# Optimization experiments

Hardware: AMD Instinct MI355X
Metric: run time of the kernel (lower is better)

Reference implementation:

```python
import jax, jax.numpy as jnp
import numpy as np

B, T = 32, 1000
NN, NB, CTX = 512, 16, 64
EMB = 256
DCAT = 3 * EMB
H, L = 256, 4
PN, PB = 512, 2
S, V = 8, 64


def setup_inputs() -> dict:
    key = jax.random.key(0)
    ks = jax.random.split(key, 20)
    r = lambda i, shape, sc=1.0: jax.random.normal(ks[i], shape, dtype=jnp.float32) * sc
    nu_log = jnp.log(-jnp.log(jax.random.uniform(ks[8], (L, H), minval=0.5, maxval=0.95)))
    inp = {
        'neural_input': r(0, (B, T, NN)),
        'behavior_input': r(1, (B, T, NB)),
        'session_id': jax.random.randint(ks[2], (B,), 0, V),
        'subject_id': jax.random.randint(ks[3], (B,), 0, S),
        'session_table': r(4, (V, CTX), 0.02),
        'neural_W': r(5, (S, EMB, NN), 1.0 / np.sqrt(NN)),
        'neural_b': jnp.zeros((S, EMB), jnp.float32),
        'behavior_W': r(6, (S, EMB, NB), 1.0 / np.sqrt(NB)),
        'behavior_b': jnp.zeros((S, EMB), jnp.float32),
        'ctx_W': r(7, (EMB, CTX), 1.0 / np.sqrt(CTX)),
        'ctx_b': jnp.zeros((EMB,), jnp.float32),
        'nu_log': nu_log,
        'theta_log': jnp.log(jax.random.uniform(ks[9], (L, H), minval=1e-4, maxval=6.283)),
        'gamma_log': 0.5 * jnp.log1p(-jnp.exp(-2.0 * jnp.exp(nu_log))),
        'B_re': r(10, (L, H, DCAT), 1.0 / np.sqrt(2 * DCAT)),
        'B_im': r(11, (L, H, DCAT), 1.0 / np.sqrt(2 * DCAT)),
        'C_re': r(12, (L, DCAT, H), 1.0 / np.sqrt(H)),
        'C_im': r(13, (L, DCAT, H), 1.0 / np.sqrt(H)),
        'D_skip': r(14, (L, DCAT)),
        'dec_n_W': r(15, (S, PN, DCAT), 1.0 / np.sqrt(DCAT)),
        'dec_n_b': jnp.zeros((S, PN), jnp.float32),
        'dec_b_W': r(16, (S, PB, DCAT), 1.0 / np.sqrt(DCAT)),
        'dec_b_b': jnp.zeros((S, PB), jnp.float32),
    }
    return inp


def _lru(u, nu_log, theta_log, gamma_log, B_re, B_im, C_re, C_im, D_skip):
    # Linear Recurrent Unit: complex diagonal recurrence x_t = lam*x_{t-1} + gamma*B u_t
    lam = jnp.exp(-jnp.exp(nu_log) + 1j * jnp.exp(theta_log))  # [H]
    g = jnp.exp(gamma_log)[:, None]
    Bu = (jnp.einsum('bti,hi->bth', u, B_re * g)
          + 1j * jnp.einsum('bti,hi->bth', u, B_im * g))  # [B,T,H] complex

    def step(x, bu_t):
        x = lam * x + bu_t
        return x, x

    x0 = jnp.zeros((u.shape[0], nu_log.shape[0]), jnp.complex64)
    _, xs = jax.lax.scan(step, x0, jnp.swapaxes(Bu, 0, 1))
    xs = jnp.swapaxes(xs, 0, 1)  # [B,T,H]
    y = jnp.einsum('bth,oh->bto', xs, C_re + 1j * C_im).real + D_skip * u
    return y


def _forward(neural_input, behavior_input, session_table, neural_W, neural_b,
             behavior_W, behavior_b, ctx_W, ctx_b, nu_log, theta_log, gamma_log,
             B_re, B_im, C_re, C_im, D_skip, dec_n_W, dec_n_b, dec_b_W, dec_b_b,
             session_id, subject_id):
    act = jax.nn.relu
    Bsz, Ts, _ = neural_input.shape
    # session-token embedding -> context embedder (Linear is per-timestep, so embed once then broadcast)
    ctx = act(session_table[session_id] @ ctx_W.T + ctx_b)  # [B,EMB]
    ctx = jnp.broadcast_to(ctx[:, None, :], (Bsz, Ts, ctx.shape[-1]))
    # subject-routed embedders: gather per-sample weights, one batched GEMM
    en = act(jnp.einsum('btf,bef->bte', neural_input, neural_W[subject_id])
             + neural_b[subject_id][:, None, :])
    eb = act(jnp.einsum('btf,bef->bte', behavior_input, behavior_W[subject_id])
             + behavior_b[subject_id][:, None, :])
    h = jnp.concatenate([en, eb, ctx], axis=-1)  # [B,T,3*EMB]
    for l in range(nu_log.shape[0]):
        h = _lru(h, nu_log[l], theta_log[l], gamma_log[l],
                 B_re[l], B_im[l], C_re[l], C_im[l], D_skip[l])
    # subject-routed decoders
    pred_n = jax.nn.softplus(jnp.einsum('btd,bod->bto', h, dec_n_W[subject_id])
                             + dec_n_b[subject_id][:, None, :])
    pred_b = (jnp.einsum('btd,bod->bto', h, dec_b_W[subject_id])
              + dec_b_b[subject_id][:, None, :])
    return pred_n, pred_b


def reference(neural_input, behavior_input, session_id, subject_id, session_table,
              neural_W, neural_b, behavior_W, behavior_b, ctx_W, ctx_b,
              nu_log, theta_log, gamma_log, B_re, B_im, C_re, C_im, D_skip,
              dec_n_W, dec_n_b, dec_b_W, dec_b_b):
    return _forward(neural_input, behavior_input, session_table, neural_W, neural_b,
                    behavior_W, behavior_b, ctx_W, ctx_b, nu_log, theta_log, gamma_log,
                    B_re, B_im, C_re, C_im, D_skip, dec_n_W, dec_n_b, dec_b_W, dec_b_b,
                    session_id, subject_id)
```

## Files before the change

kernel.cpp:

```cpp
#include <hip/hip_runtime.h>

typedef __bf16 bf16;
typedef __bf16 bf16x8 __attribute__((ext_vector_type(8)));
typedef float f32x4 __attribute__((ext_vector_type(4)));

#define AS1 __attribute__((address_space(1)))
#define AS3 __attribute__((address_space(3)))

__device__ __forceinline__ void gll16(const void* g, void* l) {
    __builtin_amdgcn_global_load_lds((const AS1 void*)g, (AS3 void*)l, 16, 0, 0);
}

template<int EPI>
__global__ __launch_bounds__(512, 2)
void gemm_kern(const bf16* __restrict__ Abase, long long aBstride, int lda,
               const bf16* __restrict__ Wbase, long long wSstride,
               const float* __restrict__ biasBase, int biasStride,
               void* __restrict__ Cbase, long long cBstride, int ldc,
               const float* __restrict__ dskip,
               const bf16* __restrict__ Ubase, long long uBstride,
               const int* __restrict__ subj,
               int M, int K, int nbn)
{
    __shared__ char smem[147456];

    const int tid = threadIdx.x;
    const int lane = tid & 63;
    const int wid = tid >> 6;
    const int wm = wid >> 1, wn = wid & 1;
    const int l15 = lane & 15, lhi = lane >> 4;
    const int sw7 = l15 & 7;

    const int nwg = gridDim.x;
    const int bid = blockIdx.x;
    const int q = nwg >> 3, r = nwg & 7;
    const int xcd = bid & 7;
    const int sw = xcd * q + (xcd < r ? xcd : r) + (bid >> 3);
    const int m0 = (sw / nbn) * 256;
    const int n0 = (sw % nbn) * 128;

    const int b = blockIdx.z;
    const int s = subj ? subj[b] : 0;
    const bf16* A = Abase + (size_t)b * aBstride;
    const bf16* W = Wbase + (size_t)s * wSstride;
    const float* bias = biasBase ? biasBase + (size_t)s * biasStride : nullptr;
    const bf16* U = Ubase ? Ubase + (size_t)b * uBstride : nullptr;
    const size_t coff = (size_t)b * cBstride;
    const int Mc = M - 1;

    f32x4 acc[4][4];
    #pragma unroll
    for (int i = 0; i < 4; ++i)
        #pragma unroll
        for (int j = 0; j < 4; ++j)
            acc[i][j] = f32x4{0.f, 0.f, 0.f, 0.f};

    int rA[4], rB[4];
    #pragma unroll
    for (int f = 0; f < 4; ++f) {
        rA[f] = (wm*64 + f*16 + l15) * 128;
        rB[f] = (wn*64 + f*16 + l15) * 128;
    }

    const int sub  = tid >> 3;
    const int slot = tid & 7;
    const int ldsw = (wid << 10);

    auto stage = [&](int kt, char* buf) {
        #pragma unroll
        for (int c = 0; c < 4; ++c) {
            const int row = c*64 + sub;
            const int gk = (kt << 6) + ((slot ^ (row & 7)) << 3);
            int ar = m0 + row; if (ar > Mc) ar = Mc;
            gll16(A + (size_t)ar * lda + gk, buf + c*8192 + ldsw);
        }
        #pragma unroll
        for (int c = 0; c < 2; ++c) {
            const int row = c*64 + sub;
            const int gk = (kt << 6) + ((slot ^ (row & 7)) << 3);
            gll16(W + (size_t)(n0 + row) * K + gk, buf + 32768 + c*8192 + ldsw);
        }
    };

    char* cur = smem;
    char* nxt = smem + 49152;
    char* nn  = smem + 98304;

    const int nkt = K >> 6;
    stage(0, cur);
    if (nkt > 1) stage(1, nxt);
    asm volatile("s_waitcnt vmcnt(6)" ::: "memory");
    __builtin_amdgcn_s_barrier();

    for (int t = 0; t < nkt; ++t) {
        if (t + 2 < nkt) stage(t + 2, nn);

        #pragma unroll
        for (int kk = 0; kk < 2; ++kk) {
            const int so_ = (((kk << 2) | lhi) ^ sw7) << 4;
            bf16x8 af[4], bg[4];
            #pragma unroll
            for (int f = 0; f < 4; ++f) af[f] = *(const bf16x8*)(cur + rA[f] + so_);
            #pragma unroll
            for (int g = 0; g < 4; ++g) bg[g] = *(const bf16x8*)(cur + 32768 + rB[g] + so_);
            #pragma unroll
            for (int i = 0; i < 4; ++i)
                #pragma unroll
                for (int j = 0; j < 4; ++j)
                    acc[i][j] = __builtin_amdgcn_mfma_f32_16x16x32_bf16(
                        af[i], bg[j], acc[i][j], 0, 0, 0);
        }

        if (t + 2 < nkt) {
            asm volatile("s_waitcnt vmcnt(6)" ::: "memory");
        } else if (t + 1 < nkt) {
            asm volatile("s_waitcnt vmcnt(0)" ::: "memory");
        }
        if (t + 1 < nkt) __builtin_amdgcn_s_barrier();

        char* tmp = cur; cur = nxt; nxt = nn; nn = tmp;
    }

    __syncthreads();
    #pragma unroll
    for (int i = 0; i < 4; ++i) {
        #pragma unroll
        for (int j = 0; j < 4; ++j) {
            const int colb = (wn*64 + j*16 + l15) * 2;
            const f32x4 v = acc[i][j];
            #pragma unroll
            for (int qq = 0; qq < 4; ++qq) {
                const int row = wm*64 + i*16 + lhi*4 + qq;
                const int ad = row*256 + (colb & 15) + ((((colb >> 4) ^ (row & 7)) & 15) << 4);
                *(bf16*)(smem + ad) = (bf16)v[qq];
            }
        }
    }
    __syncthreads();

    #pragma unroll
    for (int u = 0; u < 8; ++u) {
        const int chunk = u*512 + tid;
        const int rr = chunk >> 4, ss = chunk & 15;
        const int gr = m0 + rr;
        if (gr >= M) continue;
        const int col = n0 + ss*8;
        const bf16x8 v = *(const bf16x8*)(smem + rr*256 + ((ss ^ (rr & 7)) << 4));
        if constexpr (EPI == 0) {
            const size_t ci = coff + (size_t)gr * ldc + col;
            *(bf16x8*)((bf16*)Cbase + ci) = v;
        } else if constexpr (EPI == 1) {
            const float4 b0 = *(const float4*)(bias + col);
            const float4 b1 = *(const float4*)(bias + col + 4);
            bf16x8 o;
            o[0] = (bf16)fmaxf((float)v[0] + b0.x, 0.f);
            o[1] = (bf16)fmaxf((float)v[1] + b0.y, 0.f);
            o[2] = (bf16)fmaxf((float)v[2] + b0.z, 0.f);
            o[3] = (bf16)fmaxf((float)v[3] + b0.w, 0.f);
            o[4] = (bf16)fmaxf((float)v[4] + b1.x, 0.f);
            o[5] = (bf16)fmaxf((float)v[5] + b1.y, 0.f);
            o[6] = (bf16)fmaxf((float)v[6] + b1.z, 0.f);
            o[7] = (bf16)fmaxf((float)v[7] + b1.w, 0.f);
            const size_t ci = coff + (size_t)gr * ldc + col;
            *(bf16x8*)((bf16*)Cbase + ci) = o;
        } else if constexpr (EPI == 2) {
            const bf16x8 uv = *(const bf16x8*)(U + (size_t)gr * ldc + col);
            const float4 d0 = *(const float4*)(dskip + col);
            const float4 d1 = *(const float4*)(dskip + col + 4);
            bf16x8 o;
            o[0] = (bf16)((float)v[0] + d0.x * (float)uv[0]);
            o[1] = (bf16)((float)v[1] + d0.y * (float)uv[1]);
            o[2] = (bf16)((float)v[2] + d0.z * (float)uv[2]);
            o[3] = (bf16)((float)v[3] + d0.w * (float)uv[3]);
            o[4] = (bf16)((float)v[4] + d1.x * (float)uv[4]);
            o[5] = (bf16)((float)v[5] + d1.y * (float)uv[5]);
            o[6] = (bf16)((float)v[6] + d1.z * (float)uv[6]);
            o[7] = (bf16)((float)v[7] + d1.w * (float)uv[7]);
            const size_t ci = coff + (size_t)gr * ldc + col;
            *(bf16x8*)((bf16*)Cbase + ci) = o;
        } else {
            const float4 b0 = *(const float4*)(bias + col);
            const float4 b1 = *(const float4*)(bias + col + 4);
            float xv[8];
            xv[0] = (float)v[0] + b0.x; xv[1] = (float)v[1] + b0.y;
            xv[2] = (float)v[2] + b0.z; xv[3] = (float)v[3] + b0.w;
            xv[4] = (float)v[4] + b1.x; xv[5] = (float)v[5] + b1.y;
            xv[6] = (float)v[6] + b1.z; xv[7] = (float)v[7] + b1.w;
            float4 o0, o1;
            #pragma unroll
            for (int e = 0; e < 8; ++e) {
                const float x = xv[e];
                const float sp = fmaxf(x, 0.f) + log1pf(expf(-fabsf(x)));
                if (e < 4) ((float*)&o0)[e] = sp; else ((float*)&o1)[e-4] = sp;
            }
            const size_t ci = coff + (size_t)gr * ldc + col;
            *(float4*)((float*)Cbase + ci) = o0;
            *(float4*)((float*)Cbase + ci + 4) = o1;
        }
    }
}

__global__ void scan_finals(const bf16* __restrict__ Bu,
                            const float* __restrict__ nu_log,
                            const float* __restrict__ theta_log,
                            float2* __restrict__ finals)
{
    const int g = blockIdx.x * 256 + threadIdx.x;
    const int h = g & 255;
    const int c = (g >> 8) % 20;
    const int b = g / 5120;
    const float a  = expf(nu_log[h]);
    const float th = expf(theta_log[h]);
    const float mag = expf(-a);
    const float lre = mag * cosf(th), lim = mag * sinf(th);
    float xre = 0.f, xim = 0.f;
    const bf16* p = Bu + ((size_t)(b*1000 + c*50)) * 512 + h;
    for (int i = 0; i < 50; ++i) {
        const float bre = (float)p[0], bim = (float)p[256];
        const float nre = lre*xre - lim*xim + bre;
        const float nim = lre*xim + lim*xre + bim;
        xre = nre; xim = nim;
        p += 512;
    }
    finals[(b*20 + c)*256 + h] = make_float2(xre, xim);
}

__global__ void scan_carry(const float2* __restrict__ finals,
                           float2* __restrict__ carry,
                           const float* __restrict__ nu_log,
                           const float* __restrict__ theta_log)
{
    const int g = blockIdx.x * 256 + threadIdx.x;
    const int h = g & 255;
    const int b = g >> 8;
    const float a  = expf(nu_log[h]);
    const float th = expf(theta_log[h]);
    const float mag = expf(-50.f * a);
    const float ang = 50.f * th;
    const float cre = mag * cosf(ang), cim = mag * sinf(ang);
    float pre = 0.f, pim = 0.f;
    for (int c = 0; c < 20; ++c) {
        const int idx = (b*20 + c)*256 + h;
        carry[idx] = make_float2(pre, pim);
        const float2 f = finals[idx];
        const float nre = f.x + cre*pre - cim*pim;
        const float nim = f.y + cre*pim + cim*pre;
        pre = nre; pim = nim;
    }
}

__global__ void scan_emit(const bf16* __restrict__ Bu,
                          const float2* __restrict__ carry,
                          const float* __restrict__ nu_log,
                          const float* __restrict__ theta_log,
                          bf16* __restrict__ xs)
{
    const int g = blockIdx.x * 256 + threadIdx.x;
    const int h = g & 255;
    const int c = (g >> 8) % 20;
    const int b = g / 5120;
    const float a  = expf(nu_log[h]);
    const float th = expf(theta_log[h]);
    const float mag = expf(-a);
    const float lre = mag * cosf(th), lim = mag * sinf(th);
    const float2 cr = carry[(b*20 + c)*256 + h];
    float xre = cr.x, xim = cr.y;
    const bf16* p = Bu + ((size_t)(b*1000 + c*50)) * 512 + h;
    bf16* qp = xs + ((size_t)(b*1000 + c*50)) * 512 + h;
    for (int i = 0; i < 50; ++i) {
        const float bre = (float)p[0], bim = (float)p[256];
        const float nre = lre*xre - lim*xim + bre;
        const float nim = lre*xim + lim*xre + bim;
        xre = nre; xim = nim;
        qp[0] = (bf16)xre; qp[256] = (bf16)xim;
        p += 512; qp += 512;
    }
}

__global__ void cast8_kern(const float* __restrict__ src, bf16* __restrict__ dst, int n8)
{
    const int i = blockIdx.x * 256 + threadIdx.x;
    if (i >= n8) return;
    const float4* s = (const float4*)src + (size_t)i*2;
    const float4 v0 = s[0], v1 = s[1];
    bf16x8 o;
    o[0] = (bf16)v0.x; o[1] = (bf16)v0.y; o[2] = (bf16)v0.z; o[3] = (bf16)v0.w;
    o[4] = (bf16)v1.x; o[5] = (bf16)v1.y; o[6] = (bf16)v1.z; o[7] = (bf16)v1.w;
    *((bf16x8*)dst + i) = o;
}

__global__ void packWB_kern(const float* __restrict__ Bre, const float* __restrict__ Bim,
                            const float* __restrict__ glog, bf16* __restrict__ WB)
{
    const int idx = blockIdx.x * 256 + threadIdx.x;
    if (idx >= 4*512*768) return;
    const int l = idx / (512*768);
    const int r = idx - l*(512*768);
    const int n = r / 768;
    const int k = r - n*768;
    float v;
    if (n < 256) v = Bre[((size_t)(l*256 + n))*768 + k] * expf(glog[l*256 + n]);
    else         v = Bim[((size_t)(l*256 + (n-256)))*768 + k] * expf(glog[l*256 + (n-256)]);
    WB[idx] = (bf16)v;
}

__global__ void packWC_kern(const float* __restrict__ Cre, const float* __restrict__ Cim,
                            bf16* __restrict__ WC)
{
    const int idx = blockIdx.x * 256 + threadIdx.x;
    if (idx >= 4*768*512) return;
    const int l = idx / (768*512);
    const int r = idx - l*(768*512);
    const int o = r / 512;
    const int k = r - o*512;
    const float v = (k < 256) ? Cre[((size_t)(l*768 + o))*256 + k]
                              : -Cim[((size_t)(l*768 + o))*256 + (k - 256)];
    WC[idx] = (bf16)v;
}

__global__ void ctx_kern(const float* __restrict__ st, const int* __restrict__ sess,
                         const float* __restrict__ cW, const float* __restrict__ cb,
                         float* __restrict__ ctx)
{
    const int b = blockIdx.x;
    const int e = threadIdx.x;
    const int sid = sess[b];
    const float* r = st + (size_t)sid * 64;
    const float* w = cW + (size_t)e * 64;
    float acc = cb[e];
    #pragma unroll 8
    for (int i = 0; i < 64; ++i) acc += r[i] * w[i];
    ctx[b*256 + e] = fmaxf(acc, 0.f);
}

__global__ void ebctx_kern(const float* __restrict__ behav,
                           const float* __restrict__ bW,
                           const float* __restrict__ bB,
                           const int* __restrict__ subj,
                           const float* __restrict__ ctx,
                           bf16* __restrict__ h0)
{
    const int blk = blockIdx.x;
    const int b = blk / 1000;
    const int e = threadIdx.x;
    __shared__ float binp[16];
    if (e < 16) binp[e] = behav[(size_t)blk*16 + e];
    __syncthreads();
    const int s = subj[b];
    const float* w = bW + ((size_t)(s*256) + e)*16;
    float acc = bB[s*256 + e];
    #pragma unroll
    for (int i = 0; i < 16; ++i) acc += binp[i] * w[i];
    acc = fmaxf(acc, 0.f);
    bf16* hp = h0 + (size_t)blk * 768;
    hp[256 + e] = (bf16)acc;
    hp[512 + e] = (bf16)ctx[b*256 + e];
}

__global__ void predb_kern(const bf16* __restrict__ h, const float* __restrict__ W,
                           const float* __restrict__ bb, const int* __restrict__ subj,
                           float* __restrict__ out)
{
    const int lane = threadIdx.x & 63;
    const int wid  = threadIdx.x >> 6;
    const int row  = blockIdx.x * 4 + wid;
    const int b = row / 1000;
    const int s = subj[b];
    const bf16* hr = h + (size_t)row * 768;
    const float* w0 = W + (size_t)(s*2) * 768;
    const float* w1 = w0 + 768;
    float a0 = 0.f, a1 = 0.f;
    #pragma unroll
    for (int j = 0; j < 12; ++j) {
        const int idx = j*64 + lane;
        const float hv = (float)hr[idx];
        a0 += hv * w0[idx];
        a1 += hv * w1[idx];
    }
    #pragma unroll
    for (int m = 32; m >= 1; m >>= 1) {
        a0 += __shfl_xor(a0, m);
        a1 += __shfl_xor(a1, m);
    }
    if (lane == 0) {
        out[(size_t)row*2 + 0] = a0 + bb[s*2 + 0];
        out[(size_t)row*2 + 1] = a1 + bb[s*2 + 1];
    }
}

extern "C" void kernel_launch(void* const* d_in, const int* in_sizes, int n_in,
                              void* d_out, int out_size, void* d_ws, size_t ws_size,
                              hipStream_t stream)
{
    const float* neural_input   = (const float*)d_in[0];
    const float* behavior_input = (const float*)d_in[1];
    const int*   session_id     = (const int*)d_in[2];
    const int*   subject_id     = (const int*)d_in[3];
    const float* session_table  = (const float*)d_in[4];
    const float* neural_W  = (const float*)d_in[5];
    const float* neural_b  = (const float*)d_in[6];
    const float* behavior_W = (const float*)d_in[7];
    const float* behavior_b = (const float*)d_in[8];
    const float* ctx_W = (const float*)d_in[9];
    const float* ctx_b = (const float*)d_in[10];
    const float* nu_log    = (const float*)d_in[11];
    const float* theta_log = (const float*)d_in[12];
    const float* gamma_log = (const float*)d_in[13];
    const float* B_re = (const float*)d_in[14];
    const float* B_im = (const float*)d_in[15];
    const float* C_re = (const float*)d_in[16];
    const float* C_im = (const float*)d_in[17];
    const float* D_skip = (const float*)d_in[18];
    const float* dec_n_W = (const float*)d_in[19];
    const float* dec_n_b = (const float*)d_in[20];
    const float* dec_b_W = (const float*)d_in[21];
    const float* dec_b_b = (const float*)d_in[22];
    float* out = (float*)d_out;

    char* ws = (char*)d_ws;
    size_t off = 0;
    auto alloc = [&](size_t bytes) -> char* {
        char* p = ws + off;
        off += (bytes + 255) & ~(size_t)255;
        return p;
    };
    bf16*   Wn      = (bf16*)alloc((size_t)8*256*512*2);
    bf16*   Wd      = (bf16*)alloc((size_t)8*512*768*2);
    bf16*   WB      = (bf16*)alloc((size_t)4*512*768*2);
    bf16*   WC      = (bf16*)alloc((size_t)4*768*512*2);
    float*  ctxbuf  = (float*)alloc((size_t)32*256*4);
    bf16*   hA      = (bf16*)alloc((size_t)32*1000*768*2);
    bf16*   hB      = (bf16*)alloc((size_t)32*1000*768*2);
    bf16*   xs      = (bf16*)alloc((size_t)32*1000*512*2);
    float2* finals  = (float2*)alloc((size_t)32*20*256*8);
    float2* carry   = (float2*)alloc((size_t)32*20*256*8);
    bf16*   Bu      = (bf16*)alloc((size_t)32*1000*512*2);
    bf16*   nbf     = Bu;

    cast8_kern<<<dim3(512),   256, 0, stream>>>(neural_W, Wn, 131072);
    cast8_kern<<<dim3(1536),  256, 0, stream>>>(dec_n_W,  Wd, 393216);
    packWB_kern<<<dim3(6144), 256, 0, stream>>>(B_re, B_im, gamma_log, WB);
    packWC_kern<<<dim3(6144), 256, 0, stream>>>(C_re, C_im, WC);
    ctx_kern<<<dim3(32), 256, 0, stream>>>(session_table, session_id, ctx_W, ctx_b, ctxbuf);
    cast8_kern<<<dim3(8000), 256, 0, stream>>>(neural_input, nbf, 2048000);

    ebctx_kern<<<dim3(32000), 256, 0, stream>>>(behavior_input, behavior_W, behavior_b,
                                                subject_id, ctxbuf, hA);
    gemm_kern<1><<<dim3(8, 1, 32), 512, 0, stream>>>(
        nbf, 512000LL, 512, Wn, 131072LL, neural_b, 256,
        hA, 768000LL, 768, nullptr, nullptr, 0LL, subject_id, 1000, 512, 2);

    for (int l = 0; l < 4; ++l) {
        const bf16* hin  = (l & 1) ? hB : hA;
        bf16*       hout = (l & 1) ? hA : hB;
        gemm_kern<0><<<dim3(500, 1, 1), 512, 0, stream>>>(
            hin, 0LL, 768, WB + (size_t)l*393216, 0LL, nullptr, 0,
            Bu, 0LL, 512, nullptr, nullptr, 0LL, nullptr, 32000, 768, 4);
        scan_finals<<<dim3(640), 256, 0, stream>>>(Bu, nu_log + l*256, theta_log + l*256, finals);
        scan_carry<<<dim3(32), 256, 0, stream>>>(finals, carry, nu_log + l*256, theta_log + l*256);
        scan_emit<<<dim3(640), 256, 0, stream>>>(Bu, carry, nu_log + l*256, theta_log + l*256, xs);
        gemm_kern<2><<<dim3(750, 1, 1), 512, 0, stream>>>(
            xs, 0LL, 512, WC + (size_t)l*393216, 0LL, nullptr, 0,
            hout, 0LL, 768, D_skip + l*768, hin, 0LL, nullptr, 32000, 512, 6);
    }

    gemm_kern<3><<<dim3(16, 1, 32), 512, 0, stream>>>(
        hA, 768000LL, 768, Wd, 393216LL, dec_n_b, 512,
        out, 512000LL, 512, nullptr, nullptr, 0LL, subject_id, 1000, 768, 4);
    predb_kern<<<dim3(8000), 256, 0, stream>>>(hA, dec_b_W, dec_b_b, subject_id,
                                               out + 16384000);
}
```

Measured before the change: 606.4 us.

## Split scan into finer chunks, batch behavior embedding, use offset-based GEMM buffers

The chunked LRU scan now uses 40 chunks of 25 steps instead of 20 of 50, doubling the thread count in the finals and emit kernels to shorten each serial chain. The carry pass lengthens to 40 steps. The behavior-embedding kernel now launches 256 blocks that keep the weights in registers and loop over 125 timesteps each, replacing one block per timestep. The GEMM kernel becomes a device body with named per-epilogue wrappers and integer buffer offsets in place of rotating pointers, which may change register allocation.

```diff
diff --git a/kernel.cpp b/kernel.cpp
--- a/kernel.cpp
+++ b/kernel.cpp
@@ -12,18 +12,16 @@
 }
 
 template<int EPI>
-__global__ __launch_bounds__(512, 2)
-void gemm_kern(const bf16* __restrict__ Abase, long long aBstride, int lda,
+__device__ __forceinline__
+void gemm_body(const bf16* __restrict__ Abase, long long aBstride, int lda,
                const bf16* __restrict__ Wbase, long long wSstride,
                const float* __restrict__ biasBase, int biasStride,
                void* __restrict__ Cbase, long long cBstride, int ldc,
                const float* __restrict__ dskip,
                const bf16* __restrict__ Ubase, long long uBstride,
                const int* __restrict__ subj,
-               int M, int K, int nbn)
-{
-    __shared__ char smem[147456];
-
+               int M, int K, int nbn, char* smem)
+{
     const int tid = threadIdx.x;
     const int lane = tid & 63;
     const int wid = tid >> 6;
@@ -66,43 +64,41 @@
     const int slot = tid & 7;
     const int ldsw = (wid << 10);
 
-    auto stage = [&](int kt, char* buf) {
+    auto stage = [&](int kt, int bufo) {
         #pragma unroll
         for (int c = 0; c < 4; ++c) {
             const int row = c*64 + sub;
             const int gk = (kt << 6) + ((slot ^ (row & 7)) << 3);
             int ar = m0 + row; if (ar > Mc) ar = Mc;
-            gll16(A + (size_t)ar * lda + gk, buf + c*8192 + ldsw);
+            gll16(A + (size_t)ar * lda + gk, smem + bufo + c*8192 + ldsw);
         }
         #pragma unroll
         for (int c = 0; c < 2; ++c) {
             const int row = c*64 + sub;
             const int gk = (kt << 6) + ((slot ^ (row & 7)) << 3);
-            gll16(W + (size_t)(n0 + row) * K + gk, buf + 32768 + c*8192 + ldsw);
+            gll16(W + (size_t)(n0 + row) * K + gk, smem + bufo + 32768 + c*8192 + ldsw);
         }
     };
 
-    char* cur = smem;
-    char* nxt = smem + 49152;
-    char* nn  = smem + 98304;
-
     const int nkt = K >> 6;
-    stage(0, cur);
-    if (nkt > 1) stage(1, nxt);
+    stage(0, 0);
+    if (nkt > 1) stage(1, 49152);
     asm volatile("s_waitcnt vmcnt(6)" ::: "memory");
     __builtin_amdgcn_s_barrier();
 
+    int curo = 0, nno = 98304;
     for (int t = 0; t < nkt; ++t) {
-        if (t + 2 < nkt) stage(t + 2, nn);
-
+        if (t + 2 < nkt) stage(t + 2, nno);
+
+        const char* cb = smem + curo;
         #pragma unroll
         for (int kk = 0; kk < 2; ++kk) {
             const int so_ = (((kk << 2) | lhi) ^ sw7) << 4;
             bf16x8 af[4], bg[4];
             #pragma unroll
-            for (int f = 0; f < 4; ++f) af[f] = *(const bf16x8*)(cur + rA[f] + so_);
+            for (int f = 0; f < 4; ++f) af[f] = *(const bf16x8*)(cb + rA[f] + so_);
             #pragma unroll
-            for (int g = 0; g < 4; ++g) bg[g] = *(const bf16x8*)(cur + 32768 + rB[g] + so_);
+            for (int g = 0; g < 4; ++g) bg[g] = *(const bf16x8*)(cb + 32768 + rB[g] + so_);
             #pragma unroll
             for (int i = 0; i < 4; ++i)
                 #pragma unroll
@@ -118,7 +114,8 @@
         }
         if (t + 1 < nkt) __builtin_amdgcn_s_barrier();
 
-        char* tmp = cur; cur = nxt; nxt = nn; nn = tmp;
+        curo = (curo == 98304) ? 0 : curo + 49152;
+        nno  = (nno  == 98304) ? 0 : nno  + 49152;
     }
 
     __syncthreads();
@@ -200,6 +197,26 @@
     }
 }
 
+#define GEMM_WRAP(NAME, EPI)                                                     \
+__global__ __launch_bounds__(512, 2)                                             \
+void NAME(const bf16* __restrict__ Abase, long long aBstride, int lda,           \
+          const bf16* __restrict__ Wbase, long long wSstride,                    \
+          const float* __restrict__ biasBase, int biasStride,                    \
+          void* __restrict__ Cbase, long long cBstride, int ldc,                 \
+          const float* __restrict__ dskip,                                       \
+          const bf16* __restrict__ Ubase, long long uBstride,                    \
+          const int* __restrict__ subj, int M, int K, int nbn)                   \
+{                                                                                \
+    __shared__ char smem[147456];                                                \
+    gemm_body<EPI>(Abase, aBstride, lda, Wbase, wSstride, biasBase, biasStride,  \
+                   Cbase, cBstride, ldc, dskip, Ubase, uBstride, subj,           \
+                   M, K, nbn, smem);                                             \
+}
+GEMM_WRAP(gemm_en,  1)
+GEMM_WRAP(gemm_bu,  0)
+GEMM_WRAP(gemm_y,   2)
+GEMM_WRAP(gemm_dec, 3)
+
 __global__ void scan_finals(const bf16* __restrict__ Bu,
                             const float* __restrict__ nu_log,
                             const float* __restrict__ theta_log,
@@ -207,22 +224,22 @@
 {
     const int g = blockIdx.x * 256 + threadIdx.x;
     const int h = g & 255;
-    const int c = (g >> 8) % 20;
-    const int b = g / 5120;
+    const int c = (g >> 8) % 40;
+    const int b = g / 10240;
     const float a  = expf(nu_log[h]);
     const float th = expf(theta_log[h]);
     const float mag = expf(-a);
     const float lre = mag * cosf(th), lim = mag * sinf(th);
     float xre = 0.f, xim = 0.f;
-    const bf16* p = Bu + ((size_t)(b*1000 + c*50)) * 512 + h;
-    for (int i = 0; i < 50; ++i) {
+    const bf16* p = Bu + ((size_t)(b*1000 + c*25)) * 512 + h;
+    for (int i = 0; i < 25; ++i) {
         const float bre = (float)p[0], bim = (float)p[256];
         const float nre = lre*xre - lim*xim + bre;
         const float nim = lre*xim + lim*xre + bim;
         xre = nre; xim = nim;
         p += 512;
     }
-    finals[(b*20 + c)*256 + h] = make_float2(xre, xim);
+    finals[(b*40 + c)*256 + h] = make_float2(xre, xim);
 }
 
 __global__ void scan_carry(const float2* __restrict__ finals,
@@ -235,12 +252,12 @@
     const int b = g >> 8;
     const float a  = expf(nu_log[h]);
     const float th = expf(theta_log[h]);
-    const float mag = expf(-50.f * a);
-    const float ang = 50.f * th;
+    const float mag = expf(-25.f * a);
+    const float ang = 25.f * th;
     const float cre = mag * cosf(ang), cim = mag * sinf(ang);
     float pre = 0.f, pim = 0.f;
-    for (int c = 0; c < 20; ++c) {
-        const int idx = (b*20 + c)*256 + h;
+    for (int c = 0; c < 40; ++c) {
+        const int idx = (b*40 + c)*256 + h;
         carry[idx] = make_float2(pre, pim);
         const float2 f = finals[idx];
         const float nre = f.x + cre*pre - cim*pim;
@@ -257,17 +274,17 @@
 {
     const int g = blockIdx.x * 256 + threadIdx.x;
     const int h = g & 255;
-    const int c = (g >> 8) % 20;
-    const int b = g / 5120;
+    const int c = (g >> 8) % 40;
+    const int b = g / 10240;
     const float a  = expf(nu_log[h]);
     const float th = expf(theta_log[h]);
     const float mag = expf(-a);
     const float lre = mag * cosf(th), lim = mag * sinf(th);
-    const float2 cr = carry[(b*20 + c)*256 + h];
+    const float2 cr = carry[(b*40 + c)*256 + h];
     float xre = cr.x, xim = cr.y;
-    const bf16* p = Bu + ((size_t)(b*1000 + c*50)) * 512 + h;
-    bf16* qp = xs + ((size_t)(b*1000 + c*50)) * 512 + h;
-    for (int i = 0; i < 50; ++i) {
+    const bf16* p = Bu + ((size_t)(b*1000 + c*25)) * 512 + h;
+    bf16* qp = xs + ((size_t)(b*1000 + c*25)) * 512 + h;
+    for (int i = 0; i < 25; ++i) {
         const float bre = (float)p[0], bim = (float)p[256];
         const float nre = lre*xre - lim*xim + bre;
         const float nim = lre*xim + lim*xre + bim;
@@ -340,21 +357,27 @@
                            const float* __restrict__ ctx,
                            bf16* __restrict__ h0)
 {
-    const int blk = blockIdx.x;
-    const int b = blk / 1000;
+    const int b  = blockIdx.x >> 3;
+    const int tc = blockIdx.x & 7;
     const int e = threadIdx.x;
-    __shared__ float binp[16];
-    if (e < 16) binp[e] = behav[(size_t)blk*16 + e];
-    __syncthreads();
     const int s = subj[b];
+    float wreg[16];
     const float* w = bW + ((size_t)(s*256) + e)*16;
-    float acc = bB[s*256 + e];
-    #pragma unroll
-    for (int i = 0; i < 16; ++i) acc += binp[i] * w[i];
-    acc = fmaxf(acc, 0.f);
-    bf16* hp = h0 + (size_t)blk * 768;
-    hp[256 + e] = (bf16)acc;
-    hp[512 + e] = (bf16)ctx[b*256 + e];
+    #pragma unroll
+    for (int i = 0; i < 16; ++i) wreg[i] = w[i];
+    const float bb_ = bB[s*256 + e];
+    const bf16 cx = (bf16)ctx[b*256 + e];
+    const int t0 = tc * 125;
+    for (int t = t0; t < t0 + 125; ++t) {
+        const int blk = b*1000 + t;
+        const float* bi = behav + (size_t)blk * 16;
+        float acc = bb_;
+        #pragma unroll
+        for (int i = 0; i < 16; ++i) acc += bi[i] * wreg[i];
+        bf16* hp = h0 + (size_t)blk * 768;
+        hp[256 + e] = (bf16)fmaxf(acc, 0.f);
+        hp[512 + e] = cx;
+    }
 }
 
 __global__ void predb_kern(const bf16* __restrict__ h, const float* __restrict__ W,
@@ -432,8 +455,8 @@
     bf16*   hA      = (bf16*)alloc((size_t)32*1000*768*2);
     bf16*   hB      = (bf16*)alloc((size_t)32*1000*768*2);
     bf16*   xs      = (bf16*)alloc((size_t)32*1000*512*2);
-    float2* finals  = (float2*)alloc((size_t)32*20*256*8);
-    float2* carry   = (float2*)alloc((size_t)32*20*256*8);
+    float2* finals  = (float2*)alloc((size_t)32*40*256*8);
+    float2* carry   = (float2*)alloc((size_t)32*40*256*8);
     bf16*   Bu      = (bf16*)alloc((size_t)32*1000*512*2);
     bf16*   nbf     = Bu;
 
@@ -444,27 +467,27 @@
     ctx_kern<<<dim3(32), 256, 0, stream>>>(session_table, session_id, ctx_W, ctx_b, ctxbuf);
     cast8_kern<<<dim3(8000), 256, 0, stream>>>(neural_input, nbf, 2048000);
 
-    ebctx_kern<<<dim3(32000), 256, 0, stream>>>(behavior_input, behavior_W, behavior_b,
-                                                subject_id, ctxbuf, hA);
-    gemm_kern<1><<<dim3(8, 1, 32), 512, 0, stream>>>(
+    ebctx_kern<<<dim3(256), 256, 0, stream>>>(behavior_input, behavior_W, behavior_b,
+                                              subject_id, ctxbuf, hA);
+    gemm_en<<<dim3(8, 1, 32), 512, 0, stream>>>(
         nbf, 512000LL, 512, Wn, 131072LL, neural_b, 256,
         hA, 768000LL, 768, nullptr, nullptr, 0LL, subject_id, 1000, 512, 2);
 
     for (int l = 0; l < 4; ++l) {
         const bf16* hin  = (l & 1) ? hB : hA;
         bf16*       hout = (l & 1) ? hA : hB;
-        gemm_kern<0><<<dim3(500, 1, 1), 512, 0, stream>>>(
+        gemm_bu<<<dim3(500, 1, 1), 512, 0, stream>>>(
             hin, 0LL, 768, WB + (size_t)l*393216, 0LL, nullptr, 0,
             Bu, 0LL, 512, nullptr, nullptr, 0LL, nullptr, 32000, 768, 4);
-        scan_finals<<<dim3(640), 256, 0, stream>>>(Bu, nu_log + l*256, theta_log + l*256, finals);
+        scan_finals<<<dim3(1280), 256, 0, stream>>>(Bu, nu_log + l*256, theta_log + l*256, finals);
         scan_carry<<<dim3(32), 256, 0, stream>>>(finals, carry, nu_log + l*256, theta_log + l*256);
-        scan_emit<<<dim3(640), 256, 0, stream>>>(Bu, carry, nu_log + l*256, theta_log + l*256, xs);
-        gemm_kern<2><<<dim3(750, 1, 1), 512, 0, stream>>>(
+        scan_emit<<<dim3(1280), 256, 0, stream>>>(Bu, carry, nu_log + l*256, theta_log + l*256, xs);
+        gemm_y<<<dim3(750, 1, 1), 512, 0, stream>>>(
             xs, 0LL, 512, WC + (size_t)l*393216, 0LL, nullptr, 0,
             hout, 0LL, 768, D_skip + l*768, hin, 0LL, nullptr, 32000, 512, 6);
     }
 
-    gemm_kern<3><<<dim3(16, 1, 32), 512, 0, stream>>>(
+    gemm_dec<<<dim3(16, 1, 32), 512, 0, stream>>>(
         hA, 768000LL, 768, Wd, 393216LL, dec_n_b, 512,
         out, 512000LL, 512, nullptr, nullptr, 0LL, subject_id, 1000, 768, 4);
     predb_kern<<<dim3(8000), 256, 0, stream>>>(hA, dec_b_W, dec_b_b, subject_id,
```

New measurement: 610.6 us. Within noise of the previous version (+0.7%).
